# Kernel tuning notes

Hardware: AMD Instinct MI355X
Metric: run time of the kernel (lower is better)

## Reference

```python
import jax, jax.numpy as jnp
import numpy as np

N = 100000   # nodes
E = 3200000  # edges (avg degree 32)
F = 128      # feature dim
K = 10       # propagation order (hardcoded in module)


def setup_inputs() -> dict:
    key = jax.random.key(0)
    k1, k2 = jax.random.split(key, 2)
    x = jax.random.normal(k1, (N, F), dtype=jnp.float32)
    edge_index = jax.random.randint(k2, (2, E), 0, N, dtype=jnp.int32)
    mf_weights = jnp.ones((1, K + 1, 1), dtype=jnp.float32)
    # coef_upd='none' with alpha=0.5 -> lap_coefs init = min(1/0.5, 1.0) = 1.0, frozen
    lap_coefs = jnp.ones((K + 1,), dtype=jnp.float32)
    return {"x": x, "mf_weights": mf_weights, "lap_coefs": lap_coefs,
            "edge_index": edge_index}


def reference(x, mf_weights, lap_coefs, edge_index):
    n = x.shape[0]
    row, col = edge_index[0], edge_index[1]
    # gcn_norm without self loops: deg over destination (col), symmetric norm
    deg = jax.ops.segment_sum(jnp.ones((edge_index.shape[1],), x.dtype), col,
                              num_segments=n)
    dinv = jnp.where(deg > 0, jax.lax.rsqrt(jnp.maximum(deg, 1.0)) * jnp.where(deg > 0, jnp.ones_like(deg), 0.0), 0.0)
    dinv = jnp.where(deg > 0, deg ** -0.5, 0.0)
    norm = dinv[row] * dinv[col]  # [E]

    def prop(h):  # out[col] += norm * h[row]  (scatter-add SpMM)
        return jax.ops.segment_sum(norm[:, None] * h[row], col, num_segments=n)

    # Chebyshev-like recurrence: An=2, Bn=0, Cn=-1 -> P_i = 2*prop(P_{i-1}) - P_{i-2}
    outs = [x, prop(x)]
    for i in range(2, K + 1):
        outs.append(2.0 * prop(outs[-1]) - outs[-2])

    # coef_outs[0] = P0/1 ; coef_outs[i] = lap_coefs[i-1]/1 * P_i (norm_weights all 1)
    coef = jnp.concatenate([jnp.ones((1,), x.dtype), lap_coefs[:K]])  # [K+1]
    stacked = jnp.stack(outs, axis=1)  # [N, K+1, F]
    ret = jnp.sum(stacked * coef[None, :, None] * mf_weights, axis=1)  # [N, F]
    return ret
```

## Files before the change

kernel.cpp:

```cpp
#include <hip/hip_runtime.h>
#include <hip/hip_bf16.h>
#include <hip/hip_fp16.h>

#define FDIM 128

typedef float f4 __attribute__((ext_vector_type(4)));


__global__ void degree_kernel(const int* __restrict__ col, int* __restrict__ deg, int E) {
    int e = blockIdx.x * blockDim.x + threadIdx.x;
    if (e < E) atomicAdd(&deg[col[e]], 1);
}

__global__ void dinv_kernel(const int* __restrict__ deg, float* __restrict__ dinv, int N) {
    int i = blockIdx.x * blockDim.x + threadIdx.x;
    if (i < N) {
        int d = deg[i];
        dinv[i] = (d > 0) ? rsqrtf((float)d) : 0.0f;
    }
}


__global__ void scan_blocks_kernel(const int* __restrict__ deg, int* __restrict__ rowptr,
                                   int* __restrict__ bsum, int N) {
    __shared__ int s[256];
    int t = threadIdx.x;
    int i = blockIdx.x * 256 + t;
    int v = (i < N) ? deg[i] : 0;
    s[t] = v;
    __syncthreads();
    for (int off = 1; off < 256; off <<= 1) {
        int add = (t >= off) ? s[t - off] : 0;
        __syncthreads();
        s[t] += add;
        __syncthreads();
    }
    if (i < N) rowptr[i] = s[t] - v;
    if (t == 255) bsum[blockIdx.x] = s[255];
}

__global__ void scan_bsums_kernel(int* __restrict__ bsum, int* __restrict__ boff, int nb) {
    __shared__ int s[512];
    int t = threadIdx.x;
    int v = (t < nb) ? bsum[t] : 0;
    s[t] = v;
    __syncthreads();
    for (int off = 1; off < 512; off <<= 1) {
        int add = (t >= off) ? s[t - off] : 0;
        __syncthreads();
        s[t] += add;
        __syncthreads();
    }
    if (t < nb) boff[t] = s[t] - v;
}

__global__ void add_offsets_kernel(int* __restrict__ rowptr, int* __restrict__ cursor,
                                   const int* __restrict__ boff, int N, int E) {
    int i = blockIdx.x * blockDim.x + threadIdx.x;
    if (i < N) {
        int v = rowptr[i] + boff[i >> 8];
        rowptr[i] = v;
        cursor[i] = v;
    }
    if (i == 0) rowptr[N] = E;
}


__global__ void place_kernel(const int* __restrict__ row, const int* __restrict__ col,
                             const float* __restrict__ dinv, int* __restrict__ cursor,
                             float2* __restrict__ edata, int E) {
    int e = blockIdx.x * blockDim.x + threadIdx.x;
    if (e < E) {
        int r = row[e], c = col[e];
        float w = dinv[r] * dinv[c];
        int pos = atomicAdd(&cursor[c], 1);
        edata[pos] = make_float2(__int_as_float(r), w);
    }
}


__global__ void init_out_kernel(const float4* __restrict__ x, const float* __restrict__ mf,
                                float4* __restrict__ out, float4* __restrict__ hx, long n8) {
    long i = (long)blockIdx.x * blockDim.x + threadIdx.x;
    if (i < n8) {
        float w = mf[0];
        float4 a = x[2 * i];
        float4 b = x[2 * i + 1];
        out[2 * i]     = make_float4(w * a.x, w * a.y, w * a.z, w * a.w);
        out[2 * i + 1] = make_float4(w * b.x, w * b.y, w * b.z, w * b.w);
        __half2 h[4];
        h[0] = __floats2half2_rn(a.x, a.y);
        h[1] = __floats2half2_rn(a.z, a.w);
        h[2] = __floats2half2_rn(b.x, b.y);
        h[3] = __floats2half2_rn(b.z, b.w);
        hx[i] = *(const float4*)h;
    }
}


__global__ __launch_bounds__(256) void gather_prop_kernel(
        const float2* __restrict__ edata, const int* __restrict__ rowptr,
        const __half* __restrict__ src, const float* __restrict__ prev2,
        float* __restrict__ tgt, __half* __restrict__ tgth, float* __restrict__ out,
        const float* __restrict__ mf, const float* __restrict__ lap,
        int i_coef, float scale, float beta, int N) {
    int wid = blockIdx.x * 4 + (threadIdx.x >> 6);
    if (wid >= N) return;
    int lane = threadIdx.x & 63;
    int g  = lane >> 4;
    int fl = lane & 15;
    int feoff = fl << 3;

    int begin = rowptr[wid];
    int end   = rowptr[wid + 1];

    float acc[8];
    #pragma unroll
    for (int j = 0; j < 8; ++j) acc[j] = 0.f;

    #pragma unroll 4
    for (int e0 = begin; e0 < end; e0 += 4) {
        int e = e0 + g;
        float w = 0.f;
        int idx = 0;
        if (e < end) {
            float2 ed = edata[e];
            idx = __float_as_int(ed.x);
            w = ed.y;
        }
        f4 raw = *(const f4*)(src + ((long)idx << 7) + feoff);
        const __half2* h = (const __half2*)&raw;
        float2 f0 = __half22float2(h[0]);
        float2 f1 = __half22float2(h[1]);
        float2 f2 = __half22float2(h[2]);
        float2 f3 = __half22float2(h[3]);
        acc[0] += w * f0.x; acc[1] += w * f0.y;
        acc[2] += w * f1.x; acc[3] += w * f1.y;
        acc[4] += w * f2.x; acc[5] += w * f2.y;
        acc[6] += w * f3.x; acc[7] += w * f3.y;
    }

    #pragma unroll
    for (int j = 0; j < 8; ++j) {
        acc[j] += __shfl_xor(acc[j], 16, 64);
        acc[j] += __shfl_xor(acc[j], 32, 64);
    }

    if (g == 0) {
        float coef = mf[i_coef] * lap[i_coef - 1];
        long o = ((long)wid << 7) + feoff;
        float r[8];
        if (beta != 0.f) {
            f4 p0 = __builtin_nontemporal_load((const f4*)(prev2 + o));
            f4 p1 = __builtin_nontemporal_load((const f4*)(prev2 + o) + 1);
            r[0] = scale * acc[0] + beta * p0.x;
            r[1] = scale * acc[1] + beta * p0.y;
            r[2] = scale * acc[2] + beta * p0.z;
            r[3] = scale * acc[3] + beta * p0.w;
            r[4] = scale * acc[4] + beta * p1.x;
            r[5] = scale * acc[5] + beta * p1.y;
            r[6] = scale * acc[6] + beta * p1.z;
            r[7] = scale * acc[7] + beta * p1.w;
        } else {
            #pragma unroll
            for (int j = 0; j < 8; ++j) r[j] = scale * acc[j];
        }
        f4 t0 = {r[0], r[1], r[2], r[3]};
        f4 t1 = {r[4], r[5], r[6], r[7]};
        __builtin_nontemporal_store(t0, (f4*)(tgt + o));
        __builtin_nontemporal_store(t1, (f4*)(tgt + o) + 1);
        if (tgth) {
            __half2 hh[4];
            hh[0] = __floats2half2_rn(r[0], r[1]);
            hh[1] = __floats2half2_rn(r[2], r[3]);
            hh[2] = __floats2half2_rn(r[4], r[5]);
            hh[3] = __floats2half2_rn(r[6], r[7]);
            __builtin_nontemporal_store(*(const f4*)hh, (f4*)(tgth + o));
        }
        f4 o0 = __builtin_nontemporal_load((const f4*)(out + o));
        f4 o1 = __builtin_nontemporal_load((const f4*)(out + o) + 1);
        o0.x += coef * r[0]; o0.y += coef * r[1]; o0.z += coef * r[2]; o0.w += coef * r[3];
        o1.x += coef * r[4]; o1.y += coef * r[5]; o1.z += coef * r[6]; o1.w += coef * r[7];
        __builtin_nontemporal_store(o0, (f4*)(out + o));
        __builtin_nontemporal_store(o1, (f4*)(out + o) + 1);
    }
}

extern "C" void kernel_launch(void* const* d_in, const int* in_sizes, int n_in,
                              void* d_out, int out_size, void* d_ws, size_t ws_size,
                              hipStream_t stream) {
    const float* x   = (const float*)d_in[0];
    const float* mf  = (const float*)d_in[1];
    const float* lap = (const float*)d_in[2];
    const int*   ei  = (const int*)d_in[3];
    float* out = (float*)d_out;

    const int  K  = in_sizes[1] - 1;
    const long NF = (long)in_sizes[0];
    const int  N  = (int)(NF / FDIM);
    const int  E  = in_sizes[3] / 2;
    const int* row = ei;
    const int* col = ei + E;

    char* wp = (char*)d_ws;
    float*  bufA   = (float*)wp;  wp += NF * sizeof(float);
    float*  bufB   = (float*)wp;  wp += NF * sizeof(float);
    __half* hbufA  = (__half*)wp; wp += NF * sizeof(__half);
    __half* hbufB  = (__half*)wp; wp += NF * sizeof(__half);
    float2* edata  = (float2*)wp; wp += (size_t)E * sizeof(float2);
    int*    rowptr = (int*)wp;    wp += (size_t)(N + 1) * sizeof(int);
    int*    cursor = (int*)wp;    wp += (size_t)N * sizeof(int);
    int*    deg    = (int*)wp;    wp += (size_t)N * sizeof(int);
    float*  dinv   = (float*)wp;  wp += (size_t)N * sizeof(float);
    int*    bsum   = (int*)wp;    wp += 512 * sizeof(int);
    int*    boff   = (int*)wp;    wp += 512 * sizeof(int);

    const int BT = 256;
    const long n8 = NF / 8;
    const int n8_blocks = (int)((n8 + BT - 1) / BT);
    const int e_blocks  = (E + BT - 1) / BT;
    const int n_blocks  = (N + BT - 1) / BT;

    hipMemsetAsync(deg, 0, (size_t)N * sizeof(int), stream);
    degree_kernel<<<e_blocks, BT, 0, stream>>>(col, deg, E);
    dinv_kernel<<<n_blocks, BT, 0, stream>>>(deg, dinv, N);
    scan_blocks_kernel<<<n_blocks, BT, 0, stream>>>(deg, rowptr, bsum, N);
    scan_bsums_kernel<<<1, 512, 0, stream>>>(bsum, boff, n_blocks);
    add_offsets_kernel<<<n_blocks, BT, 0, stream>>>(rowptr, cursor, boff, N, E);
    place_kernel<<<e_blocks, BT, 0, stream>>>(row, col, dinv, cursor, edata, E);

    init_out_kernel<<<n8_blocks, BT, 0, stream>>>((const float4*)x, mf, (float4*)out,
                                                  (float4*)hbufB, n8);

    const int g_blocks = (N + 3) / 4;

    gather_prop_kernel<<<g_blocks, BT, 0, stream>>>(edata, rowptr, hbufB, x,
                                                    bufA, hbufA, out, mf, lap,
                                                    1, 1.0f, 0.0f, N);
    for (int i = 2; i <= K; ++i) {
        const __half* srch  = (i % 2 == 0) ? hbufA : hbufB;
        float*        tgt   = (i % 2 == 0) ? bufB : bufA;
        __half*       tgth  = (i % 2 == 0) ? hbufB : hbufA;
        const float*  prev2 = (i == 2) ? x : (const float*)tgt;
        if (i == K) tgth = nullptr;
        gather_prop_kernel<<<g_blocks, BT, 0, stream>>>(edata, rowptr, srch, prev2,
                                                        tgt, tgth, out, mf, lap,
                                                        i, 2.0f, -1.0f, N);
    }
}
```

Baseline: 1.783 ms.

## Split half-precision features into per-XCD chunks for L2-resident gathers

```diff
diff --git a/kernel.cpp b/kernel.cpp
--- a/kernel.cpp
+++ b/kernel.cpp
@@ -3,8 +3,11 @@
 #include <hip/hip_fp16.h>
 
 #define FDIM 128
+#define NCHUNK 8
+#define CF 16
 
 typedef float f4 __attribute__((ext_vector_type(4)));
+typedef float f2v __attribute__((ext_vector_type(2)));
 
 
 __global__ void degree_kernel(const int* __restrict__ col, int* __restrict__ deg, int E) {
@@ -80,7 +83,8 @@
 
 
 __global__ void init_out_kernel(const float4* __restrict__ x, const float* __restrict__ mf,
-                                float4* __restrict__ out, float4* __restrict__ hx, long n8) {
+                                float4* __restrict__ out, __half* __restrict__ hx,
+                                int N, long n8) {
     long i = (long)blockIdx.x * blockDim.x + threadIdx.x;
     if (i < n8) {
         float w = mf[0];
@@ -93,7 +97,11 @@
         h[1] = __floats2half2_rn(a.z, a.w);
         h[2] = __floats2half2_rn(b.x, b.y);
         h[3] = __floats2half2_rn(b.z, b.w);
-        hx[i] = *(const float4*)h;
+        long n  = i >> 4;
+        int  f0 = (int)(i & 15) * 8;
+        int  c  = f0 >> 4;
+        long haddr = ((long)c * N + n) * CF + (f0 & 15);
+        *(f4*)(hx + haddr) = *(const f4*)h;
     }
 }
 
@@ -104,85 +112,67 @@
         float* __restrict__ tgt, __half* __restrict__ tgth, float* __restrict__ out,
         const float* __restrict__ mf, const float* __restrict__ lap,
         int i_coef, float scale, float beta, int N) {
-    int wid = blockIdx.x * 4 + (threadIdx.x >> 6);
-    if (wid >= N) return;
-    int lane = threadIdx.x & 63;
-    int g  = lane >> 4;
-    int fl = lane & 15;
-    int feoff = fl << 3;
-
-    int begin = rowptr[wid];
-    int end   = rowptr[wid + 1];
-
-    float acc[8];
-    #pragma unroll
-    for (int j = 0; j < 8; ++j) acc[j] = 0.f;
-
-    #pragma unroll 4
-    for (int e0 = begin; e0 < end; e0 += 4) {
-        int e = e0 + g;
-        float w = 0.f;
-        int idx = 0;
-        if (e < end) {
-            float2 ed = edata[e];
-            idx = __float_as_int(ed.x);
-            w = ed.y;
+    const int c    = blockIdx.x & 7;
+    const int wave = threadIdx.x >> 6;
+    const int lane = threadIdx.x & 63;
+    const int eg   = lane >> 3;
+    const int fg   = lane & 7;
+    const long cN  = (long)c * N;
+    const float coef = mf[i_coef] * lap[i_coef - 1];
+
+    int d0 = (blockIdx.x >> 3) * 32 + wave * 8;
+
+    for (int di = 0; di < 8; ++di) {
+        int d = d0 + di;
+        if (d >= N) return;
+        int begin = rowptr[d];
+        int end   = rowptr[d + 1];
+
+        float ax = 0.f, ay = 0.f;
+        #pragma unroll 4
+        for (int e0 = begin; e0 < end; e0 += 8) {
+            int e = e0 + eg;
+            float w = 0.f;
+            int idx = 0;
+            if (e < end) {
+                f2v ed = __builtin_nontemporal_load((const f2v*)edata + e);
+                idx = __float_as_int(ed.x);
+                w = ed.y;
+            }
+            const __half2 v = *(const __half2*)(src + ((cN + idx) << 4) + (fg << 1));
+            float2 vf = __half22float2(v);
+            ax += w * vf.x;
+            ay += w * vf.y;
         }
-        f4 raw = *(const f4*)(src + ((long)idx << 7) + feoff);
-        const __half2* h = (const __half2*)&raw;
-        float2 f0 = __half22float2(h[0]);
-        float2 f1 = __half22float2(h[1]);
-        float2 f2 = __half22float2(h[2]);
-        float2 f3 = __half22float2(h[3]);
-        acc[0] += w * f0.x; acc[1] += w * f0.y;
-        acc[2] += w * f1.x; acc[3] += w * f1.y;
-        acc[4] += w * f2.x; acc[5] += w * f2.y;
-        acc[6] += w * f3.x; acc[7] += w * f3.y;
-    }
-
-    #pragma unroll
-    for (int j = 0; j < 8; ++j) {
-        acc[j] += __shfl_xor(acc[j], 16, 64);
-        acc[j] += __shfl_xor(acc[j], 32, 64);
-    }
-
-    if (g == 0) {
-        float coef = mf[i_coef] * lap[i_coef - 1];
-        long o = ((long)wid << 7) + feoff;
-        float r[8];
-        if (beta != 0.f) {
-            f4 p0 = __builtin_nontemporal_load((const f4*)(prev2 + o));
-            f4 p1 = __builtin_nontemporal_load((const f4*)(prev2 + o) + 1);
-            r[0] = scale * acc[0] + beta * p0.x;
-            r[1] = scale * acc[1] + beta * p0.y;
-            r[2] = scale * acc[2] + beta * p0.z;
-            r[3] = scale * acc[3] + beta * p0.w;
-            r[4] = scale * acc[4] + beta * p1.x;
-            r[5] = scale * acc[5] + beta * p1.y;
-            r[6] = scale * acc[6] + beta * p1.z;
-            r[7] = scale * acc[7] + beta * p1.w;
-        } else {
-            #pragma unroll
-            for (int j = 0; j < 8; ++j) r[j] = scale * acc[j];
+
+        ax += __shfl_xor(ax, 8, 64);
+        ay += __shfl_xor(ay, 8, 64);
+        ax += __shfl_xor(ax, 16, 64);
+        ay += __shfl_xor(ay, 16, 64);
+        ax += __shfl_xor(ax, 32, 64);
+        ay += __shfl_xor(ay, 32, 64);
+
+        if (lane < 8) {
+            long o = ((long)d << 7) + (c << 4) + (fg << 1);
+            float rx, ry;
+            if (beta != 0.f) {
+                f2v p = __builtin_nontemporal_load((const f2v*)(prev2 + o));
+                rx = scale * ax + beta * p.x;
+                ry = scale * ay + beta * p.y;
+            } else {
+                rx = scale * ax;
+                ry = scale * ay;
+            }
+            f2v t = {rx, ry};
+            __builtin_nontemporal_store(t, (f2v*)(tgt + o));
+            if (tgth) {
+                *(__half2*)(tgth + ((cN + d) << 4) + (fg << 1)) = __floats2half2_rn(rx, ry);
+            }
+            f2v ov = __builtin_nontemporal_load((const f2v*)(out + o));
+            ov.x += coef * rx;
+            ov.y += coef * ry;
+            __builtin_nontemporal_store(ov, (f2v*)(out + o));
         }
-        f4 t0 = {r[0], r[1], r[2], r[3]};
-        f4 t1 = {r[4], r[5], r[6], r[7]};
-        __builtin_nontemporal_store(t0, (f4*)(tgt + o));
-        __builtin_nontemporal_store(t1, (f4*)(tgt + o) + 1);
-        if (tgth) {
-            __half2 hh[4];
-            hh[0] = __floats2half2_rn(r[0], r[1]);
-            hh[1] = __floats2half2_rn(r[2], r[3]);
-            hh[2] = __floats2half2_rn(r[4], r[5]);
-            hh[3] = __floats2half2_rn(r[6], r[7]);
-            __builtin_nontemporal_store(*(const f4*)hh, (f4*)(tgth + o));
-        }
-        f4 o0 = __builtin_nontemporal_load((const f4*)(out + o));
-        f4 o1 = __builtin_nontemporal_load((const f4*)(out + o) + 1);
-        o0.x += coef * r[0]; o0.y += coef * r[1]; o0.z += coef * r[2]; o0.w += coef * r[3];
-        o1.x += coef * r[4]; o1.y += coef * r[5]; o1.z += coef * r[6]; o1.w += coef * r[7];
-        __builtin_nontemporal_store(o0, (f4*)(out + o));
-        __builtin_nontemporal_store(o1, (f4*)(out + o) + 1);
     }
 }
 
@@ -230,9 +220,9 @@
     place_kernel<<<e_blocks, BT, 0, stream>>>(row, col, dinv, cursor, edata, E);
 
     init_out_kernel<<<n8_blocks, BT, 0, stream>>>((const float4*)x, mf, (float4*)out,
-                                                  (float4*)hbufB, n8);
-
-    const int g_blocks = (N + 3) / 4;
+                                                  hbufB, N, n8);
+
+    const int g_blocks = 8 * ((N + 31) / 32);
 
     gather_prop_kernel<<<g_blocks, BT, 0, stream>>>(edata, rowptr, hbufB, x,
                                                     bufA, hbufA, out, mf, lap,
```

New measurement: 5.664 ms. +217.6%, slower.

## Feature-chunk the half-precision source and fold edge weights into dinv prescaling

Applied to the files above, without the earlier changes.

```diff
diff --git a/kernel.cpp b/kernel.cpp
--- a/kernel.cpp
+++ b/kernel.cpp
@@ -3,6 +3,7 @@
 #include <hip/hip_fp16.h>
 
 #define FDIM 128
+#define CF 16
 
 typedef float f4 __attribute__((ext_vector_type(4)));
 
@@ -67,20 +68,20 @@
 
 
 __global__ void place_kernel(const int* __restrict__ row, const int* __restrict__ col,
-                             const float* __restrict__ dinv, int* __restrict__ cursor,
-                             float2* __restrict__ edata, int E) {
+                             int* __restrict__ cursor, int* __restrict__ eidx, int E) {
     int e = blockIdx.x * blockDim.x + threadIdx.x;
     if (e < E) {
-        int r = row[e], c = col[e];
-        float w = dinv[r] * dinv[c];
+        int c = col[e];
         int pos = atomicAdd(&cursor[c], 1);
-        edata[pos] = make_float2(__int_as_float(r), w);
+        eidx[pos] = row[e];
     }
 }
 
 
 __global__ void init_out_kernel(const float4* __restrict__ x, const float* __restrict__ mf,
-                                float4* __restrict__ out, float4* __restrict__ hx, long n8) {
+                                const float* __restrict__ dinv,
+                                float4* __restrict__ out, __half* __restrict__ hx,
+                                int N, long n8) {
     long i = (long)blockIdx.x * blockDim.x + threadIdx.x;
     if (i < n8) {
         float w = mf[0];
@@ -88,102 +89,113 @@
         float4 b = x[2 * i + 1];
         out[2 * i]     = make_float4(w * a.x, w * a.y, w * a.z, w * a.w);
         out[2 * i + 1] = make_float4(w * b.x, w * b.y, w * b.z, w * b.w);
+        long n  = i >> 4;
+        int  f0 = (int)(i & 15) * 8;
+        float dv = dinv[n];
         __half2 h[4];
-        h[0] = __floats2half2_rn(a.x, a.y);
-        h[1] = __floats2half2_rn(a.z, a.w);
-        h[2] = __floats2half2_rn(b.x, b.y);
-        h[3] = __floats2half2_rn(b.z, b.w);
-        hx[i] = *(const float4*)h;
+        h[0] = __floats2half2_rn(dv * a.x, dv * a.y);
+        h[1] = __floats2half2_rn(dv * a.z, dv * a.w);
+        h[2] = __floats2half2_rn(dv * b.x, dv * b.y);
+        h[3] = __floats2half2_rn(dv * b.z, dv * b.w);
+        long haddr = ((long)(f0 >> 4) * N + n) * CF + (f0 & 8);
+        *(f4*)(hx + haddr) = *(const f4*)h;
     }
 }
 
 
 __global__ __launch_bounds__(256) void gather_prop_kernel(
-        const float2* __restrict__ edata, const int* __restrict__ rowptr,
+        const int* __restrict__ eidx, const int* __restrict__ rowptr,
+        const float* __restrict__ dinv,
         const __half* __restrict__ src, const float* __restrict__ prev2,
         float* __restrict__ tgt, __half* __restrict__ tgth, float* __restrict__ out,
         const float* __restrict__ mf, const float* __restrict__ lap,
         int i_coef, float scale, float beta, int N) {
-    int wid = blockIdx.x * 4 + (threadIdx.x >> 6);
-    if (wid >= N) return;
-    int lane = threadIdx.x & 63;
-    int g  = lane >> 4;
-    int fl = lane & 15;
-    int feoff = fl << 3;
-
-    int begin = rowptr[wid];
-    int end   = rowptr[wid + 1];
+    const int c    = blockIdx.x & 7;
+    const int wave = threadIdx.x >> 6;
+    const int lane = threadIdx.x & 63;
+    const int dloc = lane >> 1;
+    const int fg   = lane & 1;
+    const long cN  = (long)c * N;
+
+    int d = (blockIdx.x >> 3) * 128 + wave * 32 + dloc;
+    bool valid = d < N;
+    int begin = 0, nit = 0;
+    if (valid) {
+        begin = rowptr[d];
+        nit   = rowptr[d + 1] - begin;
+    }
+    int maxit = nit;
+    #pragma unroll
+    for (int m = 2; m <= 32; m <<= 1)
+        maxit = max(maxit, __shfl_xor(maxit, m, 64));
 
     float acc[8];
     #pragma unroll
     for (int j = 0; j < 8; ++j) acc[j] = 0.f;
 
+    const __half* srcc = src + (cN << 4) + (fg << 3);
+
     #pragma unroll 4
-    for (int e0 = begin; e0 < end; e0 += 4) {
-        int e = e0 + g;
-        float w = 0.f;
+    for (int k = 0; k < maxit; ++k) {
         int idx = 0;
-        if (e < end) {
-            float2 ed = edata[e];
-            idx = __float_as_int(ed.x);
-            w = ed.y;
+        float wsel = 0.f;
+        if (k < nit) {
+            idx = eidx[begin + k];
+            wsel = 1.f;
         }
-        f4 raw = *(const f4*)(src + ((long)idx << 7) + feoff);
+        f4 raw = *(const f4*)(srcc + ((long)idx << 4));
         const __half2* h = (const __half2*)&raw;
         float2 f0 = __half22float2(h[0]);
         float2 f1 = __half22float2(h[1]);
         float2 f2 = __half22float2(h[2]);
         float2 f3 = __half22float2(h[3]);
-        acc[0] += w * f0.x; acc[1] += w * f0.y;
-        acc[2] += w * f1.x; acc[3] += w * f1.y;
-        acc[4] += w * f2.x; acc[5] += w * f2.y;
-        acc[6] += w * f3.x; acc[7] += w * f3.y;
-    }
-
-    #pragma unroll
-    for (int j = 0; j < 8; ++j) {
-        acc[j] += __shfl_xor(acc[j], 16, 64);
-        acc[j] += __shfl_xor(acc[j], 32, 64);
-    }
-
-    if (g == 0) {
-        float coef = mf[i_coef] * lap[i_coef - 1];
-        long o = ((long)wid << 7) + feoff;
-        float r[8];
-        if (beta != 0.f) {
-            f4 p0 = __builtin_nontemporal_load((const f4*)(prev2 + o));
-            f4 p1 = __builtin_nontemporal_load((const f4*)(prev2 + o) + 1);
-            r[0] = scale * acc[0] + beta * p0.x;
-            r[1] = scale * acc[1] + beta * p0.y;
-            r[2] = scale * acc[2] + beta * p0.z;
-            r[3] = scale * acc[3] + beta * p0.w;
-            r[4] = scale * acc[4] + beta * p1.x;
-            r[5] = scale * acc[5] + beta * p1.y;
-            r[6] = scale * acc[6] + beta * p1.z;
-            r[7] = scale * acc[7] + beta * p1.w;
-        } else {
-            #pragma unroll
-            for (int j = 0; j < 8; ++j) r[j] = scale * acc[j];
-        }
-        f4 t0 = {r[0], r[1], r[2], r[3]};
-        f4 t1 = {r[4], r[5], r[6], r[7]};
-        __builtin_nontemporal_store(t0, (f4*)(tgt + o));
-        __builtin_nontemporal_store(t1, (f4*)(tgt + o) + 1);
-        if (tgth) {
-            __half2 hh[4];
-            hh[0] = __floats2half2_rn(r[0], r[1]);
-            hh[1] = __floats2half2_rn(r[2], r[3]);
-            hh[2] = __floats2half2_rn(r[4], r[5]);
-            hh[3] = __floats2half2_rn(r[6], r[7]);
-            __builtin_nontemporal_store(*(const f4*)hh, (f4*)(tgth + o));
-        }
-        f4 o0 = __builtin_nontemporal_load((const f4*)(out + o));
-        f4 o1 = __builtin_nontemporal_load((const f4*)(out + o) + 1);
-        o0.x += coef * r[0]; o0.y += coef * r[1]; o0.z += coef * r[2]; o0.w += coef * r[3];
-        o1.x += coef * r[4]; o1.y += coef * r[5]; o1.z += coef * r[6]; o1.w += coef * r[7];
-        __builtin_nontemporal_store(o0, (f4*)(out + o));
-        __builtin_nontemporal_store(o1, (f4*)(out + o) + 1);
-    }
+        acc[0] += wsel * f0.x; acc[1] += wsel * f0.y;
+        acc[2] += wsel * f1.x; acc[3] += wsel * f1.y;
+        acc[4] += wsel * f2.x; acc[5] += wsel * f2.y;
+        acc[6] += wsel * f3.x; acc[7] += wsel * f3.y;
+    }
+
+    if (!valid) return;
+
+    float dv   = dinv[d];
+    float sdv  = scale * dv;
+    float coef = mf[i_coef] * lap[i_coef - 1];
+    long  o    = ((long)d << 7) + (c << 4) + (fg << 3);
+
+    float r[8];
+    if (beta != 0.f) {
+        f4 p0 = __builtin_nontemporal_load((const f4*)(prev2 + o));
+        f4 p1 = __builtin_nontemporal_load((const f4*)(prev2 + o) + 1);
+        r[0] = sdv * acc[0] + beta * p0.x;
+        r[1] = sdv * acc[1] + beta * p0.y;
+        r[2] = sdv * acc[2] + beta * p0.z;
+        r[3] = sdv * acc[3] + beta * p0.w;
+        r[4] = sdv * acc[4] + beta * p1.x;
+        r[5] = sdv * acc[5] + beta * p1.y;
+        r[6] = sdv * acc[6] + beta * p1.z;
+        r[7] = sdv * acc[7] + beta * p1.w;
+    } else {
+        #pragma unroll
+        for (int j = 0; j < 8; ++j) r[j] = sdv * acc[j];
+    }
+    f4 t0 = {r[0], r[1], r[2], r[3]};
+    f4 t1 = {r[4], r[5], r[6], r[7]};
+    __builtin_nontemporal_store(t0, (f4*)(tgt + o));
+    __builtin_nontemporal_store(t1, (f4*)(tgt + o) + 1);
+    if (tgth) {
+        __half2 hh[4];
+        hh[0] = __floats2half2_rn(dv * r[0], dv * r[1]);
+        hh[1] = __floats2half2_rn(dv * r[2], dv * r[3]);
+        hh[2] = __floats2half2_rn(dv * r[4], dv * r[5]);
+        hh[3] = __floats2half2_rn(dv * r[6], dv * r[7]);
+        *(f4*)(tgth + ((cN + d) << 4) + (fg << 3)) = *(const f4*)hh;
+    }
+    f4 o0 = __builtin_nontemporal_load((const f4*)(out + o));
+    f4 o1 = __builtin_nontemporal_load((const f4*)(out + o) + 1);
+    o0.x += coef * r[0]; o0.y += coef * r[1]; o0.z += coef * r[2]; o0.w += coef * r[3];
+    o1.x += coef * r[4]; o1.y += coef * r[5]; o1.z += coef * r[6]; o1.w += coef * r[7];
+    __builtin_nontemporal_store(o0, (f4*)(out + o));
+    __builtin_nontemporal_store(o1, (f4*)(out + o) + 1);
 }
 
 extern "C" void kernel_launch(void* const* d_in, const int* in_sizes, int n_in,
@@ -207,7 +219,7 @@
     float*  bufB   = (float*)wp;  wp += NF * sizeof(float);
     __half* hbufA  = (__half*)wp; wp += NF * sizeof(__half);
     __half* hbufB  = (__half*)wp; wp += NF * sizeof(__half);
-    float2* edata  = (float2*)wp; wp += (size_t)E * sizeof(float2);
+    int*    eidx   = (int*)wp;    wp += (size_t)E * sizeof(int);
     int*    rowptr = (int*)wp;    wp += (size_t)(N + 1) * sizeof(int);
     int*    cursor = (int*)wp;    wp += (size_t)N * sizeof(int);
     int*    deg    = (int*)wp;    wp += (size_t)N * sizeof(int);
@@ -227,14 +239,14 @@
     scan_blocks_kernel<<<n_blocks, BT, 0, stream>>>(deg, rowptr, bsum, N);
     scan_bsums_kernel<<<1, 512, 0, stream>>>(bsum, boff, n_blocks);
     add_offsets_kernel<<<n_blocks, BT, 0, stream>>>(rowptr, cursor, boff, N, E);
-    place_kernel<<<e_blocks, BT, 0, stream>>>(row, col, dinv, cursor, edata, E);
-
-    init_out_kernel<<<n8_blocks, BT, 0, stream>>>((const float4*)x, mf, (float4*)out,
-                                                  (float4*)hbufB, n8);
-
-    const int g_blocks = (N + 3) / 4;
-
-    gather_prop_kernel<<<g_blocks, BT, 0, stream>>>(edata, rowptr, hbufB, x,
+    place_kernel<<<e_blocks, BT, 0, stream>>>(row, col, cursor, eidx, E);
+
+    init_out_kernel<<<n8_blocks, BT, 0, stream>>>((const float4*)x, mf, dinv,
+                                                  (float4*)out, hbufB, N, n8);
+
+    const int g_blocks = 8 * ((N + 127) / 128);
+
+    gather_prop_kernel<<<g_blocks, BT, 0, stream>>>(eidx, rowptr, dinv, hbufB, x,
                                                     bufA, hbufA, out, mf, lap,
                                                     1, 1.0f, 0.0f, N);
     for (int i = 2; i <= K; ++i) {
@@ -243,7 +255,7 @@
         __half*       tgth  = (i % 2 == 0) ? hbufB : hbufA;
         const float*  prev2 = (i == 2) ? x : (const float*)tgt;
         if (i == K) tgth = nullptr;
-        gather_prop_kernel<<<g_blocks, BT, 0, stream>>>(edata, rowptr, srch, prev2,
+        gather_prop_kernel<<<g_blocks, BT, 0, stream>>>(eidx, rowptr, dinv, srch, prev2,
                                                         tgt, tgth, out, mf, lap,
                                                         i, 2.0f, -1.0f, N);
     }
```

After: 4.229 ms. 137% more time.

## Bin edges by destination octant before CSR placement

Applied to the files above, without the earlier changes.

```diff
diff --git a/kernel.cpp b/kernel.cpp
--- a/kernel.cpp
+++ b/kernel.cpp
@@ -66,12 +66,49 @@
 }
 
 
-__global__ void place_kernel(const int* __restrict__ row, const int* __restrict__ col,
-                             const float* __restrict__ dinv, int* __restrict__ cursor,
-                             float2* __restrict__ edata, int E) {
-    int e = blockIdx.x * blockDim.x + threadIdx.x;
-    if (e < E) {
+__global__ void octant_init_kernel(const int* __restrict__ rowptr,
+                                   int* __restrict__ gcur, int N) {
+    int o = threadIdx.x;
+    if (o < 8) gcur[o] = rowptr[(int)(((long)o * N + 7) / 8)];
+}
+
+__global__ __launch_bounds__(256) void binA_kernel(
+        const int* __restrict__ row, const int* __restrict__ col,
+        unsigned long long* __restrict__ obuf, int* __restrict__ gcur,
+        int N, int E) {
+    __shared__ int scnt[8];
+    __shared__ int sbase[8];
+    int t = threadIdx.x;
+    if (t < 8) scnt[t] = 0;
+    __syncthreads();
+    int e = blockIdx.x * 256 + t;
+    int o = 0, rank = 0;
+    unsigned long long pay = 0;
+    bool v = e < E;
+    if (v) {
         int r = row[e], c = col[e];
+        o = (int)(((long)c * 8) / N);
+        pay = ((unsigned long long)(unsigned)c << 32) | (unsigned)r;
+        rank = atomicAdd(&scnt[o], 1);
+    }
+    __syncthreads();
+    if (t < 8) sbase[t] = atomicAdd(&gcur[t], scnt[t]);
+    __syncthreads();
+    if (v) obuf[sbase[o] + rank] = pay;
+}
+
+__global__ __launch_bounds__(256) void binB_kernel(
+        const unsigned long long* __restrict__ obuf, const int* __restrict__ gend,
+        const int* __restrict__ rowptr, const float* __restrict__ dinv,
+        int* __restrict__ cursor, float2* __restrict__ edata, int N, int M) {
+    int o = blockIdx.x & 7;
+    int j = blockIdx.x >> 3;
+    int sb = rowptr[(int)(((long)o * N + 7) / 8)];
+    int en = gend[o];
+    for (int p = sb + j * 256 + threadIdx.x; p < en; p += M * 256) {
+        unsigned long long pay = obuf[p];
+        int r = (int)(pay & 0xffffffffu);
+        int c = (int)(pay >> 32);
         float w = dinv[r] * dinv[c];
         int pos = atomicAdd(&cursor[c], 1);
         edata[pos] = make_float2(__int_as_float(r), w);
@@ -214,6 +251,9 @@
     float*  dinv   = (float*)wp;  wp += (size_t)N * sizeof(float);
     int*    bsum   = (int*)wp;    wp += 512 * sizeof(int);
     int*    boff   = (int*)wp;    wp += 512 * sizeof(int);
+    int*    gcur   = (int*)wp;    wp += 8 * sizeof(int);
+
+    unsigned long long* obuf = (unsigned long long*)bufA;
 
     const int BT = 256;
     const long n8 = NF / 8;
@@ -227,7 +267,10 @@
     scan_blocks_kernel<<<n_blocks, BT, 0, stream>>>(deg, rowptr, bsum, N);
     scan_bsums_kernel<<<1, 512, 0, stream>>>(bsum, boff, n_blocks);
     add_offsets_kernel<<<n_blocks, BT, 0, stream>>>(rowptr, cursor, boff, N, E);
-    place_kernel<<<e_blocks, BT, 0, stream>>>(row, col, dinv, cursor, edata, E);
+    octant_init_kernel<<<1, 8, 0, stream>>>(rowptr, gcur, N);
+    binA_kernel<<<e_blocks, BT, 0, stream>>>(row, col, obuf, gcur, N, E);
+    const int M = 256;
+    binB_kernel<<<8 * M, BT, 0, stream>>>(obuf, gcur, rowptr, dinv, cursor, edata, N, M);
 
     init_out_kernel<<<n8_blocks, BT, 0, stream>>>((const float4*)x, mf, (float4*)out,
                                                   (float4*)hbufB, n8);
```

After: 1.902 ms. 1.07x slower.
